# Performance work log

Measured on AMD Instinct MI355X. Metric: run time of the kernel, lower is better.

The kernel has to match this reference:

```python
import jax, jax.numpy as jnp
import numpy as np

B, S, D = 8, 2048, 2048
E, R, K = 8, 16, 2
NUM_TASKS, NUM_MODES = 4, 2
ALPHA = 16.0


def setup_inputs() -> dict:
    key = jax.random.key(0)
    k1, k2, k3, k4 = jax.random.split(key, 4)
    hidden_states = jax.random.normal(k1, (B, S, D), dtype=jnp.float32)
    gate_w = jax.random.normal(k2, (E, D), dtype=jnp.float32) * 0.01  # nn.init.normal_(std=0.01)
    # Soft-prior biases: fill(-1.0), strong prior 3.0 / 2.0 at configured (task, expert) / (mode, expert)
    tb = -np.ones((NUM_TASKS, E), dtype=np.float32)
    mb = -np.ones((NUM_MODES, E), dtype=np.float32)
    for e in range(E):
        tb[e % NUM_TASKS, e] = 3.0
        mb[e % NUM_MODES, e] = 2.0
    # LoRA params; lora_B is zero-init in torch but we use small random values for a nontrivial baseline
    lora_A = jax.random.normal(k3, (E, R, D), dtype=jnp.float32) * (1.0 / np.sqrt(D))
    lora_B = jax.random.normal(k4, (E, D, R), dtype=jnp.float32) * 0.02
    return {
        "hidden_states": hidden_states,
        "gate_w": gate_w,
        "task_bias": jnp.asarray(tb),
        "mode_bias": jnp.asarray(mb),
        "lora_A": lora_A,
        "lora_B": lora_B,
        "task_id": 1,
        "mode_id": 1,
    }


def reference(hidden_states, gate_w, task_bias, mode_bias, lora_A, lora_B, task_id, mode_id):
    scaling = ALPHA / R
    # Router: score = dynamic_gate(mean_pool(x)) + task_bias[t] + mode_bias[m]
    x_pooled = hidden_states.mean(axis=1)                       # [B, D]
    logits = x_pooled @ gate_w.T + task_bias[task_id] + mode_bias[mode_id]  # [B, E]
    top_v, top_i = jax.lax.top_k(logits, K)                     # [B, K]
    weights = jax.nn.softmax(top_v, axis=-1)                    # [B, K]
    # per-sample, per-expert combine weight: sum of top-k weights routed to that expert
    one_hot = jax.nn.one_hot(top_i, E, dtype=weights.dtype)     # [B, K, E]
    sw = jnp.einsum('bke,bk->be', one_hot, weights)             # [B, E]
    # LoRA experts: (x @ A_e^T) @ B_e^T * scaling, weighted-summed per sample
    mid = jnp.einsum('bsd,erd->besr', hidden_states, lora_A)    # [B, E, S, R] (small: R=16)
    out = jnp.einsum('be,besr,edr->bsd', sw, mid, lora_B) * scaling  # [B, S, D]
    return out
```

## Files before the change

### kernel.cpp

```cpp
#include <hip/hip_runtime.h>
#include <stdint.h>

typedef __attribute__((ext_vector_type(8))) short bf16x8;
typedef __attribute__((ext_vector_type(4))) float f32x4;
typedef __attribute__((ext_vector_type(16))) float f32x16;
typedef unsigned short ushort_t;

#define B_ 8
#define S_ 2048
#define D_ 2048
#define E_ 8
#define J_ 128
#define M_ 64
#define AROWS 136
#define ATILE (AROWS * 64)

static __device__ __forceinline__ unsigned short f2bf(float f) {
  union { float f; uint32_t u; } v; v.f = f;
  uint32_t u = v.u;
  return (unsigned short)((u + 0x7FFFu + ((u >> 16) & 1u)) >> 16);
}
static __device__ __forceinline__ float bf2f(ushort_t h) {
  union { uint32_t u; float f; } v; v.u = ((uint32_t)h) << 16;
  return v.f;
}
static __device__ __forceinline__ uint32_t pkbf(float a, float b) {
  uint32_t r;
  asm("v_cvt_pk_bf16_f32 %0, %1, %2" : "=v"(r) : "v"(a), "v"(b));
  return r;
}

#define GLL16(gsrc, ldst)                                                        \
  __builtin_amdgcn_global_load_lds(                                              \
      (const __attribute__((address_space(1))) void*)(gsrc),                     \
      (__attribute__((address_space(3))) void*)(ldst), 16, 0, 0)

#define SBAR() __builtin_amdgcn_sched_barrier(0)
#define VMWAIT(N)                                                                \
  do {                                                                           \
    asm volatile("s_waitcnt vmcnt(" #N ")" ::: "memory");                        \
    __builtin_amdgcn_sched_barrier(0);                                           \
  } while (0)
#define VMBAR(N)                                                                 \
  do {                                                                           \
    asm volatile("s_waitcnt vmcnt(" #N ") lgkmcnt(0)\n\ts_barrier" ::: "memory");\
    __builtin_amdgcn_sched_barrier(0);                                           \
  } while (0)

__global__ void k_prep(const float* __restrict__ lA, const float* __restrict__ lB,
                       const float* __restrict__ gw,
                       ushort_t* __restrict__ AgE, ushort_t* __restrict__ Bg) {
  int gid = blockIdx.x * blockDim.x + threadIdx.x;
  int stride = gridDim.x * blockDim.x;
  for (int o = gid; o < 32 * AROWS * 8; o += stride) {
    int kt = o / (AROWS * 8);
    int rem = o - kt * (AROWS * 8);
    int row = rem >> 3, c = rem & 7;
    int d = kt * 64 + (((c ^ row) & 7) << 3);
    const float* src = (row < 128) ? (lA + (size_t)row * D_ + d)
                                   : (gw + (size_t)(row - 128) * D_ + d);
    float4 v0 = *(const float4*)src;
    float4 v1 = *(const float4*)(src + 4);
    bf16x8 outv;
    outv[0] = (short)f2bf(v0.x); outv[1] = (short)f2bf(v0.y);
    outv[2] = (short)f2bf(v0.z); outv[3] = (short)f2bf(v0.w);
    outv[4] = (short)f2bf(v1.x); outv[5] = (short)f2bf(v1.y);
    outv[6] = (short)f2bf(v1.z); outv[7] = (short)f2bf(v1.w);
    *(bf16x8*)&AgE[(size_t)o * 8] = outv;
  }
  for (int o4 = gid; o4 < (D_ * J_) / 4; o4 += stride) {
    int j4 = o4 & 31, dd = o4 >> 5;
    int e = j4 >> 2, r0 = (j4 & 3) * 4;
    float4 v = *(const float4*)(lB + ((size_t)e * D_ + dd) * 16 + r0);
    uint2 pk;
    pk.x = (uint32_t)f2bf(v.x) | ((uint32_t)f2bf(v.y) << 16);
    pk.y = (uint32_t)f2bf(v.z) | ((uint32_t)f2bf(v.w) << 16);
    ((uint2*)Bg)[o4] = pk;
  }
}

__global__ __launch_bounds__(256) void k_mid(const float* __restrict__ x,
    const ushort_t* __restrict__ AgE, ushort_t* __restrict__ midb,
    float* __restrict__ lpart) {
  __shared__ ushort_t Ab[3][ATILE];
  __shared__ ushort_t Xb[2][M_ * 64];
  const int tid = threadIdx.x;
  const int w = tid >> 6, lane = tid & 63;
  const int l31 = lane & 31, hi = lane >> 5;
  const int jp = w & 1, sp = w >> 1;
  const int b = blockIdx.y, s0 = blockIdx.x * M_;
  const int xr = tid >> 2, xc4 = (tid & 3) * 16;
  const float* xsrc = x + ((size_t)(b * S_ + s0 + xr)) * D_ + xc4;
  const int lc0 = 2 * (tid & 3);

  f32x16 accA = {}, accB = {}, acc2 = {};

  auto stageA = [&](int buf, int kt) {
#pragma unroll
    for (int c = 0; c < 4; ++c) {
      int ch = c * 256 + tid;
      GLL16(AgE + (size_t)kt * ATILE + (size_t)ch * 8, &Ab[buf][ch * 8]);
    }
    {
      int ch = 1024 + lane;
      GLL16(AgE + (size_t)kt * ATILE + (size_t)ch * 8, &Ab[buf][(1024 + lane) * 8]);
    }
  };
  auto loadX = [&](float4* r4, int t) {
    const float* p = xsrc + t * 64;
    r4[0] = *(const float4*)(p);
    r4[1] = *(const float4*)(p + 4);
    r4[2] = *(const float4*)(p + 8);
    r4[3] = *(const float4*)(p + 12);
  };
  auto cvtWrite = [&](int buf, const float4* r4) {
    uint4 q0, q1;
    q0.x = pkbf(r4[0].x, r4[0].y); q0.y = pkbf(r4[0].z, r4[0].w);
    q0.z = pkbf(r4[1].x, r4[1].y); q0.w = pkbf(r4[1].z, r4[1].w);
    q1.x = pkbf(r4[2].x, r4[2].y); q1.y = pkbf(r4[2].z, r4[2].w);
    q1.z = pkbf(r4[3].x, r4[3].y); q1.w = pkbf(r4[3].z, r4[3].w);
    const int ph0 = lc0 ^ (xr & 7), ph1 = (lc0 + 1) ^ (xr & 7);
    *(uint4*)&Xb[buf][xr * 64 + ph0 * 8] = q0;
    *(uint4*)&Xb[buf][xr * 64 + ph1 * 8] = q1;
  };
  auto computeTile = [&](int t, int ab) {
    const int xbuf = t & 1;
    const int xrow = sp * 32 + l31;
    const int a0 = jp * 64 + l31, a1 = jp * 64 + 32 + l31, a2 = 128 + l31;
    const int rsw = (l31 & 7);
#pragma unroll
    for (int ks = 0; ks < 4; ++ks) {
      const int cc = ks * 2 + hi;
      const int chs = ((cc ^ rsw) << 3);
      bf16x8 xf = *(const bf16x8*)&Xb[xbuf][xrow * 64 + chs];
      bf16x8 af0 = *(const bf16x8*)&Ab[ab][a0 * 64 + chs];
      bf16x8 af1 = *(const bf16x8*)&Ab[ab][a1 * 64 + chs];
      accA = __builtin_amdgcn_mfma_f32_32x32x16_bf16(af0, xf, accA, 0, 0, 0);
      accB = __builtin_amdgcn_mfma_f32_32x32x16_bf16(af1, xf, accB, 0, 0, 0);
      if ((w & 1) == 0) {
        bf16x8 af2 = *(const bf16x8*)&Ab[ab][a2 * 64 + chs];
        acc2 = __builtin_amdgcn_mfma_f32_32x32x16_bf16(af2, xf, acc2, 0, 0, 0);
      }
    }
  };

  float4 xS0[4], xS1[4];
  loadX(xS0, 0); SBAR();
  stageA(0, 0);  SBAR();
  loadX(xS1, 1); SBAR();
  stageA(1, 1);  SBAR();
  VMWAIT(14);
  cvtWrite(0, xS0);
  VMBAR(9);

#define BODY(T, AB, ABN, XCUR, XNXT)                                             \
  do {                                                                           \
    loadX(XNXT, (T) + 2); SBAR();                                                \
    stageA((ABN), (T) + 2); SBAR();                                              \
    computeTile((T), (AB));                                                      \
    VMWAIT(14);                                                                  \
    cvtWrite(((T) + 1) & 1, XCUR);                                               \
    VMBAR(9);                                                                    \
  } while (0)

#pragma unroll 1
  for (int k6 = 0; k6 < 5; ++k6) {
    const int t0 = 6 * k6;
    BODY(t0 + 0, 0, 2, xS1, xS0);
    BODY(t0 + 1, 1, 0, xS0, xS1);
    BODY(t0 + 2, 2, 1, xS1, xS0);
    BODY(t0 + 3, 0, 2, xS0, xS1);
    BODY(t0 + 4, 1, 0, xS1, xS0);
    BODY(t0 + 5, 2, 1, xS0, xS1);
  }
#undef BODY
  computeTile(30, 0);
  VMWAIT(5);
  cvtWrite(1, xS1);
  VMBAR(0);
  computeTile(31, 1);

  {
    const int srow = s0 + sp * 32 + l31;
    ushort_t* mp = midb + ((size_t)(b * S_ + srow)) * J_ + jp * 64 + 4 * hi;
#pragma unroll
    for (int G = 0; G < 4; ++G) {
      uint2 pA, pB;
      pA.x = pkbf(accA[G * 4 + 0], accA[G * 4 + 1]);
      pA.y = pkbf(accA[G * 4 + 2], accA[G * 4 + 3]);
      pB.x = pkbf(accB[G * 4 + 0], accB[G * 4 + 1]);
      pB.y = pkbf(accB[G * 4 + 2], accB[G * 4 + 3]);
      *(uint2*)&mp[G * 8] = pA;
      *(uint2*)&mp[32 + G * 8] = pB;
    }
  }

  if ((w & 1) == 0) {
#pragma unroll
    for (int q = 0; q < 4; ++q) {
      float v = acc2[q];
      v += __shfl_xor(v, 1); v += __shfl_xor(v, 2);
      v += __shfl_xor(v, 4); v += __shfl_xor(v, 8);
      v += __shfl_xor(v, 16);
      if (l31 == 0)
        lpart[(((size_t)(b * 32 + blockIdx.x)) * 2 + sp) * 8 + hi * 4 + q] = v;
    }
  }
}

__global__ void k_router(const float* __restrict__ lpart,
                         const float* __restrict__ tb, const float* __restrict__ mb,
                         const int* __restrict__ task_p, const int* __restrict__ mode_p,
                         float* __restrict__ rinfo) {
  __shared__ float lg[64];
  const int t = threadIdx.x;
  const int b = t >> 3, e = t & 7;
  float s = 0.f;
  for (int k = 0; k < 64; ++k) s += lpart[((size_t)(b * 64 + k)) * 8 + e];
  lg[t] = s * (1.f / (float)S_) + tb[task_p[0] * E_ + e] + mb[mode_p[0] * E_ + e];
  __syncthreads();
  if (t < B_) {
    float v[8];
#pragma unroll
    for (int e2 = 0; e2 < 8; ++e2) v[e2] = lg[t * 8 + e2];
    int i1 = 0;
#pragma unroll
    for (int e2 = 1; e2 < 8; ++e2) if (v[e2] > v[i1]) i1 = e2;
    int i2 = (i1 == 0) ? 1 : 0;
#pragma unroll
    for (int e2 = 0; e2 < 8; ++e2) if (e2 != i1 && v[e2] > v[i2]) i2 = e2;
    float ex = __expf(v[i2] - v[i1]);
    float w1 = 1.f / (1.f + ex), w2 = ex * w1;
    float4 r;
    r.x = (float)i1; r.y = (float)i2; r.z = w1; r.w = w2;
    ((float4*)rinfo)[t] = r;
  }
}

__global__ __launch_bounds__(256) void k_comb(const ushort_t* __restrict__ midb,
    const float* __restrict__ rinfo, const ushort_t* __restrict__ Bg,
    float* __restrict__ out) {
  __shared__ ushort_t Bt[128][40];
  const int n = blockIdx.x, m = blockIdx.y, b = blockIdx.z;
  const int tid = threadIdx.x, w = tid >> 6, lane = tid & 63;
  const int lm = lane & 15, g = lane >> 4;

  const float4 ri = ((const float4*)rinfo)[b];
  const int i1 = (int)ri.x, i2 = (int)ri.y;
  const float w1 = ri.z, w2 = ri.w;

#pragma unroll
  for (int c = 0; c < 2; ++c) {
    int ci = c * 256 + tid;
    int d = ci >> 2, sub = ci & 3;
    int e = (sub & 2) ? i2 : i1;
    float sc = (sub & 2) ? w2 : w1;
    bf16x8 bv = *(const bf16x8*)(Bg + ((size_t)(n * 128 + d)) * J_ + e * 16 + (sub & 1) * 8);
    bf16x8 bw;
#pragma unroll
    for (int i = 0; i < 8; ++i) bw[i] = (short)f2bf(bf2f((ushort_t)bv[i]) * sc);
    *(bf16x8*)&Bt[d][sub * 8] = bw;
  }

  const int srow = m * 64 + w * 16 + lm;
  const int jw = (g < 2) ? (i1 * 16 + g * 8) : (i2 * 16 + (g - 2) * 8);
  bf16x8 pf = *(const bf16x8*)&midb[((size_t)(b * S_ + srow)) * J_ + jw];
  __syncthreads();

  f32x4 acc[8] = {};
#pragma unroll
  for (int nn = 0; nn < 8; ++nn) {
    bf16x8 af = *(const bf16x8*)&Bt[nn * 16 + lm][g * 8];
    acc[nn] = __builtin_amdgcn_mfma_f32_16x16x32_bf16(af, pf, acc[nn], 0, 0, 0);
  }

  float* op = out + ((size_t)(b * S_ + srow)) * D_ + n * 128;
#pragma unroll
  for (int nn = 0; nn < 8; ++nn)
    *(f32x4*)&op[nn * 16 + g * 4] = acc[nn];
}

extern "C" void kernel_launch(void* const* d_in, const int* in_sizes, int n_in,
                              void* d_out, int out_size, void* d_ws, size_t ws_size,
                              hipStream_t stream) {
  const float* x    = (const float*)d_in[0];
  const float* gw   = (const float*)d_in[1];
  const float* tb   = (const float*)d_in[2];
  const float* mb   = (const float*)d_in[3];
  const float* lA   = (const float*)d_in[4];
  const float* lB   = (const float*)d_in[5];
  const int* task_p = (const int*)d_in[6];
  const int* mode_p = (const int*)d_in[7];
  float* out = (float*)d_out;
  char* ws = (char*)d_ws;
  ushort_t* midb = (ushort_t*)ws;
  ushort_t* AgE  = (ushort_t*)(ws + 4194304);
  ushort_t* Bg   = (ushort_t*)(ws + 4751360);
  float* lpart   = (float*)(ws + 5275648);
  float* rinfo   = (float*)(ws + 5292032);

  hipLaunchKernelGGL(k_prep, dim3(256), dim3(256), 0, stream, lA, lB, gw, AgE, Bg);
  hipLaunchKernelGGL(k_mid, dim3(32, 8), dim3(256), 0, stream, x, AgE, midb, lpart);
  hipLaunchKernelGGL(k_router, dim3(1), dim3(64), 0, stream,
                     lpart, tb, mb, task_p, mode_p, rinfo);
  hipLaunchKernelGGL(k_comb, dim3(16, 32, 8), dim3(256), 0, stream, midb, rinfo, Bg, out);
}
```

Measured before the change: 80.19 us.

## Halve k_mid row tile and split K across waves with LDS reduction

k_mid now handles 32 sequence rows per block instead of 64, which doubles the grid to 512 blocks and sets launch bounds to allow two blocks per CU. The wave pairs that used to own different row halves now split each 64-wide K chunk, and their partial accumulators are combined through an LDS reduction at the end. The aim is more parallelism and occupancy for the memory-bound x stream. The cost is that the A tile is staged twice as often per row of x, plus an extra reduction pass with two block barriers.

```diff
diff --git a/kernel.cpp b/kernel.cpp
--- a/kernel.cpp
+++ b/kernel.cpp
@@ -11,7 +11,7 @@
 #define D_ 2048
 #define E_ 8
 #define J_ 128
-#define M_ 64
+#define M_ 32
 #define AROWS 136
 #define ATILE (AROWS * 64)
 
@@ -79,7 +79,7 @@
   }
 }
 
-__global__ __launch_bounds__(256) void k_mid(const float* __restrict__ x,
+__global__ __launch_bounds__(256, 2) void k_mid(const float* __restrict__ x,
     const ushort_t* __restrict__ AgE, ushort_t* __restrict__ midb,
     float* __restrict__ lpart) {
   __shared__ ushort_t Ab[3][ATILE];
@@ -87,11 +87,11 @@
   const int tid = threadIdx.x;
   const int w = tid >> 6, lane = tid & 63;
   const int l31 = lane & 31, hi = lane >> 5;
-  const int jp = w & 1, sp = w >> 1;
+  const int jp = w & 1, xi = w >> 1;
   const int b = blockIdx.y, s0 = blockIdx.x * M_;
-  const int xr = tid >> 2, xc4 = (tid & 3) * 16;
-  const float* xsrc = x + ((size_t)(b * S_ + s0 + xr)) * D_ + xc4;
-  const int lc0 = 2 * (tid & 3);
+  const int xr = tid >> 3, xc = (tid & 7) * 8;
+  const float* xsrc = x + ((size_t)(b * S_ + s0 + xr)) * D_ + xc;
+  const int xwoff = xr * 64 + (((tid & 7) ^ (xr & 7)) << 3);
 
   f32x16 accA = {}, accB = {}, acc2 = {};
 
@@ -110,57 +110,51 @@
     const float* p = xsrc + t * 64;
     r4[0] = *(const float4*)(p);
     r4[1] = *(const float4*)(p + 4);
-    r4[2] = *(const float4*)(p + 8);
-    r4[3] = *(const float4*)(p + 12);
   };
   auto cvtWrite = [&](int buf, const float4* r4) {
-    uint4 q0, q1;
-    q0.x = pkbf(r4[0].x, r4[0].y); q0.y = pkbf(r4[0].z, r4[0].w);
-    q0.z = pkbf(r4[1].x, r4[1].y); q0.w = pkbf(r4[1].z, r4[1].w);
-    q1.x = pkbf(r4[2].x, r4[2].y); q1.y = pkbf(r4[2].z, r4[2].w);
-    q1.z = pkbf(r4[3].x, r4[3].y); q1.w = pkbf(r4[3].z, r4[3].w);
-    const int ph0 = lc0 ^ (xr & 7), ph1 = (lc0 + 1) ^ (xr & 7);
-    *(uint4*)&Xb[buf][xr * 64 + ph0 * 8] = q0;
-    *(uint4*)&Xb[buf][xr * 64 + ph1 * 8] = q1;
+    uint4 q;
+    q.x = pkbf(r4[0].x, r4[0].y); q.y = pkbf(r4[0].z, r4[0].w);
+    q.z = pkbf(r4[1].x, r4[1].y); q.w = pkbf(r4[1].z, r4[1].w);
+    *(uint4*)&Xb[buf][xwoff] = q;
   };
   auto computeTile = [&](int t, int ab) {
     const int xbuf = t & 1;
-    const int xrow = sp * 32 + l31;
     const int a0 = jp * 64 + l31, a1 = jp * 64 + 32 + l31, a2 = 128 + l31;
     const int rsw = (l31 & 7);
 #pragma unroll
-    for (int ks = 0; ks < 4; ++ks) {
+    for (int k2 = 0; k2 < 2; ++k2) {
+      const int ks = xi * 2 + k2;
       const int cc = ks * 2 + hi;
       const int chs = ((cc ^ rsw) << 3);
-      bf16x8 xf = *(const bf16x8*)&Xb[xbuf][xrow * 64 + chs];
+      bf16x8 xf = *(const bf16x8*)&Xb[xbuf][l31 * 64 + chs];
       bf16x8 af0 = *(const bf16x8*)&Ab[ab][a0 * 64 + chs];
       bf16x8 af1 = *(const bf16x8*)&Ab[ab][a1 * 64 + chs];
       accA = __builtin_amdgcn_mfma_f32_32x32x16_bf16(af0, xf, accA, 0, 0, 0);
       accB = __builtin_amdgcn_mfma_f32_32x32x16_bf16(af1, xf, accB, 0, 0, 0);
-      if ((w & 1) == 0) {
+      if (jp == 0) {
         bf16x8 af2 = *(const bf16x8*)&Ab[ab][a2 * 64 + chs];
         acc2 = __builtin_amdgcn_mfma_f32_32x32x16_bf16(af2, xf, acc2, 0, 0, 0);
       }
     }
   };
 
-  float4 xS0[4], xS1[4];
+  float4 xS0[2], xS1[2];
   loadX(xS0, 0); SBAR();
   stageA(0, 0);  SBAR();
   loadX(xS1, 1); SBAR();
   stageA(1, 1);  SBAR();
-  VMWAIT(14);
+  VMWAIT(12);
   cvtWrite(0, xS0);
-  VMBAR(9);
+  VMBAR(7);
 
 #define BODY(T, AB, ABN, XCUR, XNXT)                                             \
   do {                                                                           \
     loadX(XNXT, (T) + 2); SBAR();                                                \
     stageA((ABN), (T) + 2); SBAR();                                              \
     computeTile((T), (AB));                                                      \
-    VMWAIT(14);                                                                  \
+    VMWAIT(12);                                                                  \
     cvtWrite(((T) + 1) & 1, XCUR);                                               \
-    VMBAR(9);                                                                    \
+    VMBAR(7);                                                                    \
   } while (0)
 
 #pragma unroll 1
@@ -180,9 +174,32 @@
   VMBAR(0);
   computeTile(31, 1);
 
-  {
-    const int srow = s0 + sp * 32 + l31;
-    ushort_t* mp = midb + ((size_t)(b * S_ + srow)) * J_ + jp * 64 + 4 * hi;
+  __syncthreads();
+  float* scr  = (float*)&Ab[0][0];
+  float* scr2 = (float*)&Ab[1][0];
+  if (xi == 1) {
+    float* p = scr + ((size_t)(jp * 64 + lane)) * 32;
+#pragma unroll
+    for (int G = 0; G < 4; ++G) {
+      f32x4 tA, tB;
+      tA[0] = accA[G * 4 + 0]; tA[1] = accA[G * 4 + 1];
+      tA[2] = accA[G * 4 + 2]; tA[3] = accA[G * 4 + 3];
+      tB[0] = accB[G * 4 + 0]; tB[1] = accB[G * 4 + 1];
+      tB[2] = accB[G * 4 + 2]; tB[3] = accB[G * 4 + 3];
+      *(f32x4*)&p[G * 4]      = tA;
+      *(f32x4*)&p[16 + G * 4] = tB;
+    }
+    if (jp == 0) {
+      float* p2 = scr2 + lane * 4;
+      p2[0] = acc2[0]; p2[1] = acc2[1]; p2[2] = acc2[2]; p2[3] = acc2[3];
+    }
+  }
+  __syncthreads();
+  if (xi == 0) {
+    const float* p = scr + ((size_t)(jp * 64 + lane)) * 32;
+#pragma unroll
+    for (int i = 0; i < 16; ++i) { accA[i] += p[i]; accB[i] += p[16 + i]; }
+    ushort_t* mp = midb + ((size_t)(b * S_ + s0 + l31)) * J_ + jp * 64 + 4 * hi;
 #pragma unroll
     for (int G = 0; G < 4; ++G) {
       uint2 pA, pB;
@@ -193,17 +210,17 @@
       *(uint2*)&mp[G * 8] = pA;
       *(uint2*)&mp[32 + G * 8] = pB;
     }
-  }
-
-  if ((w & 1) == 0) {
-#pragma unroll
-    for (int q = 0; q < 4; ++q) {
-      float v = acc2[q];
-      v += __shfl_xor(v, 1); v += __shfl_xor(v, 2);
-      v += __shfl_xor(v, 4); v += __shfl_xor(v, 8);
-      v += __shfl_xor(v, 16);
-      if (l31 == 0)
-        lpart[(((size_t)(b * 32 + blockIdx.x)) * 2 + sp) * 8 + hi * 4 + q] = v;
+    if (jp == 0) {
+      const float* p2 = scr2 + lane * 4;
+#pragma unroll
+      for (int q = 0; q < 4; ++q) {
+        float v = acc2[q] + p2[q];
+        v += __shfl_xor(v, 1); v += __shfl_xor(v, 2);
+        v += __shfl_xor(v, 4); v += __shfl_xor(v, 8);
+        v += __shfl_xor(v, 16);
+        if (l31 == 0)
+          lpart[((size_t)(b * 64 + blockIdx.x)) * 8 + hi * 4 + q] = v;
+      }
     }
   }
 }
@@ -300,7 +317,7 @@
   float* rinfo   = (float*)(ws + 5292032);
 
   hipLaunchKernelGGL(k_prep, dim3(256), dim3(256), 0, stream, lA, lB, gw, AgE, Bg);
-  hipLaunchKernelGGL(k_mid, dim3(32, 8), dim3(256), 0, stream, x, AgE, midb, lpart);
+  hipLaunchKernelGGL(k_mid, dim3(64, 8), dim3(256), 0, stream, x, AgE, midb, lpart);
   hipLaunchKernelGGL(k_router, dim3(1), dim3(64), 0, stream,
                      lpart, tb, mb, task_p, mode_p, rinfo);
   hipLaunchKernelGGL(k_comb, dim3(16, 32, 8), dim3(256), 0, stream, midb, rinfo, Bg, out);
```

New measurement: 84.20 us. +5.0%, slower.
